# Performance work log

Measured on AMD Instinct MI355X. Metric: run time of the kernel, lower is better.

## Reference

```python
import jax, jax.numpy as jnp
import numpy as np

N, E, C, NEF, OUT, NUM_ANGLE = 20000, 160000, 32, 1, 128, 7
F = 2 * C + NEF  # edge_fdim = 65


def setup_inputs() -> dict:
    rng = np.random.default_rng(0)
    row = rng.integers(0, N, size=E).astype(np.int32)
    col = rng.integers(0, N, size=E).astype(np.int32)
    # Line-graph incidence pairs (a, b): edge a = (i,j) feeds edge b = (j,k), i.e. col[a] == row[b].
    sort_idx = np.argsort(row, kind='stable')
    row_sorted = row[sort_idx]
    starts = np.searchsorted(row_sorted, col, 'left')
    ends = np.searchsorted(row_sorted, col, 'right')
    counts = ends - starts
    total = int(counts.sum())
    line_src = np.repeat(np.arange(E, dtype=np.int32), counts)
    base = np.repeat(starts, counts)
    within = np.arange(total, dtype=np.int64) - np.repeat(np.cumsum(counts) - counts, counts)
    line_dst = sort_idx[base + within].astype(np.int32)

    key = jax.random.key(0)
    k = jax.random.split(key, 5)
    return {
        'x': jax.random.normal(k[0], (N, C), jnp.float32),
        'edge_attr': jax.random.normal(k[1], (E, NEF), jnp.float32),
        'pos': jax.random.normal(k[2], (N, 3), jnp.float32),
        'W_msg': jax.random.normal(k[3], (OUT, NUM_ANGLE * 2 * F), jnp.float32) * 0.02,
        'b_msg': jax.random.normal(k[4], (OUT,), jnp.float32) * 0.01,
        'edge_index': jnp.asarray(np.stack([row, col]), jnp.int32),
        'line_src': jnp.asarray(line_src),
        'line_dst': jnp.asarray(line_dst),
    }


def reference(x, edge_attr, pos, W_msg, b_msg, edge_index, line_src, line_dst):
    row, col = edge_index[0], edge_index[1]
    num_node = x.shape[0]
    num_edge = row.shape[0]

    # edge_f = [x_row | x_col | edge_attr]  -> [E, F]
    edge_f = jnp.concatenate([x[row], x[col], edge_attr], axis=1)

    # Line graph: edge a=(i,j) feeds edge b=(j,k). Angle at shared node j.
    j = col[line_src]
    u = pos[row[line_src]] - pos[j]  # j -> i
    v = pos[col[line_dst]] - pos[j]  # j -> k
    cos = jnp.sum(u * v, axis=-1) / (
        jnp.linalg.norm(u, axis=-1) * jnp.linalg.norm(v, axis=-1) + 1e-8)
    ang = jnp.arccos(jnp.clip(cos, -1.0 + 1e-7, 1.0 - 1e-7))  # [0, pi]
    abin = jnp.clip((ang / jnp.pi * NUM_ANGLE).astype(jnp.int32), 0, NUM_ANGLE - 1)

    # Per target edge, accumulate neighbor-edge features into (angle bin, in/out slot).
    seg_in = line_dst.astype(jnp.int32) * (NUM_ANGLE * 2) + abin * 2      # incoming a -> b
    seg_out = line_src.astype(jnp.int32) * (NUM_ANGLE * 2) + abin * 2 + 1  # outgoing b seen from a
    vals = jnp.concatenate([edge_f[line_src], edge_f[line_dst]], axis=0)  # [2L, F]
    segs = jnp.concatenate([seg_in, seg_out], axis=0)
    msg = jax.ops.segment_sum(vals, segs, num_segments=num_edge * NUM_ANGLE * 2)
    msg = msg.reshape(num_edge, NUM_ANGLE * 2 * F)  # [E, 910]

    # output = self.message(message)  (Linear with bias)
    edge_hidden = msg @ W_msg.T + b_msg  # [E, OUT]

    # scatter_add into destination nodes (edge_index[1])
    update = jax.ops.segment_sum(edge_hidden, col, num_segments=num_node)  # [N, OUT]
    return update
```

## Files before the change

kernel.cpp:

```cpp
#include <hip/hip_runtime.h>
#include <stdint.h>

#define N_NODES 20000
#define E_EDGES 160000
#define C_DIM 32
#define OUT_DIM 128
#define K_REAL 910
#define KPH 480
#define DEG_CAP 64
#define SEG 1024
#define NSEG 20
#define MT_A (E_EDGES/256)
#define NROWS_B 20224
#define MT_B (NROWS_B/256)
#define PADW ((NROWS_B - N_NODES)*KPH/2)

typedef __attribute__((ext_vector_type(4))) float f32x4;
typedef __attribute__((ext_vector_type(8))) short short8;

__device__ __forceinline__ float bf2f(unsigned short u){
  union { unsigned int i; float f; } v; v.i = ((unsigned int)u) << 16; return v.f;
}
__device__ __forceinline__ unsigned short f2bf(float f){
  union { float f; unsigned int i; } v; v.f = f;
  unsigned int i = v.i;
  unsigned int r = (i + 0x7FFFu + ((i >> 16) & 1u)) >> 16;
  return (unsigned short)r;
}
__device__ __forceinline__ float ldv(const void* p, size_t i, int isbf){
  return isbf ? bf2f(((const unsigned short*)p)[i]) : ((const float*)p)[i];
}
__device__ __forceinline__ int clampi(int v, int hi){
  return ((unsigned)v < (unsigned)hi) ? v : 0;
}

__global__ void k_init(const void* __restrict__ xraw, int* __restrict__ flag,
                       int* __restrict__ cnt, float* __restrict__ out_acc,
                       unsigned short* __restrict__ msgN)
{
  int tid = threadIdx.x;
  if (blockIdx.x == 0){
    __shared__ int s_bad;
    if (tid == 0) s_bad = 0;
    __syncthreads();
    float v = bf2f(((const unsigned short*)xraw)[tid * 2499]);
    if (!(fabsf(v) < 100.0f)) s_bad = 1;
    __syncthreads();
    if (tid == 0) flag[0] = s_bad ? 0 : 1;
  }
  const int Z1 = 2*N_NODES;
  const int Z2 = Z1 + N_NODES*OUT_DIM;
  const int Z3 = Z2 + PADW;
  int* padp = (int*)(msgN + (size_t)N_NODES*KPH);
  for (int i = blockIdx.x*blockDim.x + tid; i < Z3; i += gridDim.x*blockDim.x){
    if (i < Z1) cnt[i] = 0;
    else if (i < Z2) ((int*)out_acc)[i - Z1] = 0;
    else padp[i - Z2] = 0;
  }
}

__global__ void k_prep(const void* __restrict__ pos, const void* __restrict__ W,
                       const int* __restrict__ row, const int* __restrict__ col,
                       float* __restrict__ vecn, int* __restrict__ cnt,
                       unsigned short* __restrict__ Wp,
                       const int* __restrict__ flg)
{
  int isbf = flg[0];
  if (blockIdx.x < MT_A){
    int e = blockIdx.x*256 + threadIdx.x;
    if (e >= E_EDGES) return;
    int r = clampi(row[e], N_NODES), c = clampi(col[e], N_NODES);
    float vx = ldv(pos, (size_t)c*3+0, isbf) - ldv(pos, (size_t)r*3+0, isbf);
    float vy = ldv(pos, (size_t)c*3+1, isbf) - ldv(pos, (size_t)r*3+1, isbf);
    float vz = ldv(pos, (size_t)c*3+2, isbf) - ldv(pos, (size_t)r*3+2, isbf);
    float nn = sqrtf(vx*vx + vy*vy + vz*vz);
    f32x4 vv; vv[0]=vx; vv[1]=vy; vv[2]=vz; vv[3]=nn;
    *(f32x4*)(vecn + (size_t)e*4) = vv;
    atomicAdd(cnt + r, 1);
    atomicAdd(cnt + N_NODES + c, 1);
  } else {
    int i = (blockIdx.x - MT_A)*256 + threadIdx.x;
    if (i >= 2*OUT_DIM*KPH) return;
    int half = i / (OUT_DIM*KPH);
    int rem = i - half*OUT_DIM*KPH;
    int o = rem / KPH, kp = rem - o*KPH;
    float v = 0.f;
    if (kp < 448){
      int t = kp >> 6, f = kp & 63;
      v = ldv(W, (size_t)o*K_REAL + (2*t + half)*65 + f, isbf);
    } else if (kp < 455){
      int t = kp - 448;
      v = ldv(W, (size_t)o*K_REAL + (2*t + half)*65 + 64, isbf);
    }
    Wp[i] = f2bf(v);
  }
}

__global__ void k_scan1(const int* __restrict__ cnt, int* __restrict__ start2,
                        int* __restrict__ segsum){
  __shared__ int buf[SEG];
  int b = blockIdx.x, arr = b / NSEG, seg = b - arr*NSEG;
  const int* cntp = cnt + (size_t)arr*N_NODES;
  int* startp = start2 + (size_t)arr*(N_NODES+1);
  int tid = threadIdx.x;
  int i = seg*SEG + tid;
  int v = (i < N_NODES) ? cntp[i] : 0;
  buf[tid] = v;
  __syncthreads();
  for (int off = 1; off < SEG; off <<= 1){
    int t = (tid >= off) ? buf[tid-off] : 0;
    __syncthreads();
    buf[tid] += t;
    __syncthreads();
  }
  if (i < N_NODES) startp[i] = buf[tid] - v;
  if (tid == SEG-1) segsum[b] = buf[tid];
}
__global__ void k_scan2(int* segsum){
  int tid = threadIdx.x;
  if (tid < 2){
    int run = 0;
    for (int s = 0; s < NSEG; ++s){
      int v = segsum[tid*NSEG+s]; segsum[tid*NSEG+s] = run; run += v;
    }
  }
}
__global__ void k_scan3(int* __restrict__ start2, int* __restrict__ fill2,
                        const int* __restrict__ segsum){
  int b = blockIdx.x, arr = b / NSEG, seg = b - arr*NSEG;
  int* startp = start2 + (size_t)arr*(N_NODES+1);
  int* fillp  = fill2  + (size_t)arr*N_NODES;
  int tid = threadIdx.x;
  int i = seg*SEG + tid;
  int add = segsum[b];
  if (i < N_NODES){ int s = startp[i] + add; startp[i] = s; fillp[i] = s; }
  if (b == 0 && tid == 0){
    start2[N_NODES] = E_EDGES;
    start2[(N_NODES+1) + N_NODES] = E_EDGES;
  }
}

__global__ void k_scatter(const int* __restrict__ row, const int* __restrict__ col,
                          int* fill2, int* list_row, int* list_col,
                          int* pos_col, int* node_of_pos)
{
  int e = blockIdx.x*blockDim.x + threadIdx.x;
  if (e >= E_EDGES) return;
  int r = clampi(row[e], N_NODES), c = clampi(col[e], N_NODES);
  int p = atomicAdd(fill2 + r, 1);
  if ((unsigned)p < E_EDGES) list_row[p] = e;
  int q = atomicAdd(fill2 + N_NODES + c, 1);
  if ((unsigned)q < E_EDGES){ list_col[q] = e; node_of_pos[q] = c; }
  pos_col[e] = clampi(q, E_EDGES);
}

__global__ __launch_bounds__(256)
void k_msg_node(const void* __restrict__ x, const void* __restrict__ eattr,
                const float* __restrict__ vecn,
                const int* __restrict__ row, const int* __restrict__ col,
                const int* __restrict__ start2,
                const int* __restrict__ list_row, const int* __restrict__ list_col,
                const int* __restrict__ pos_col,
                unsigned short* __restrict__ msg,
                uint2* __restrict__ cntb,
                const int* __restrict__ flg, int half)
{
  __shared__ int posT[DEG_CAP];
  __shared__ int othS[DEG_CAP];
  __shared__ float vS[DEG_CAP][4], vT[DEG_CAP][4];
  __shared__ float eS[DEG_CAP];
  __shared__ unsigned short fS[DEG_CAP][64];
  __shared__ float e64[DEG_CAP][8];
  __shared__ unsigned char bins[DEG_CAP][DEG_CAP];

  const float cb1 = 0.9009688679f, cb2 = 0.6234898019f, cb3 = 0.2225209340f;
  const int* start_row = start2;
  const int* start_col = start2 + (N_NODES+1);
  int j = blockIdx.x;
  int tid = threadIdx.x, wv = tid >> 6, lane = tid & 63;
  int clo = start_col[j], chi = start_col[j+1];
  int rlo = start_row[j], rhi = start_row[j+1];
  if (clo < 0) clo = 0; if (chi > E_EDGES) chi = E_EDGES; if (chi < clo) chi = clo;
  if (rlo < 0) rlo = 0; if (rhi > E_EDGES) rhi = E_EDGES; if (rhi < rlo) rhi = rlo;
  int nI = chi - clo, nO = rhi - rlo;
  int nS = half ? nO : nI;
  int nT = half ? nI : nO;
  int slo = half ? rlo : clo;
  int tlo = half ? clo : rlo;
  const int* slist = half ? list_row : list_col;
  const int* tlist = half ? list_col : list_row;
  if (nT == 0) return;
  int isbf = flg[0];

  if (nS <= DEG_CAP && nT <= DEG_CAP){
    int nS4 = (nS + 3) & ~3;
    if (tid < nS){
      int s = clampi(slist[slo+tid], E_EDGES);
      othS[tid] = clampi(half ? col[s] : row[s], N_NODES);
      eS[tid] = ldv(eattr, s, isbf);
      vS[tid][0]=vecn[s*4+0]; vS[tid][1]=vecn[s*4+1];
      vS[tid][2]=vecn[s*4+2]; vS[tid][3]=vecn[s*4+3];
    }
    if (tid < nT){
      int t = clampi(tlist[tlo+tid], E_EDGES);
      posT[tid] = clampi(pos_col[t], E_EDGES);
      vT[tid][0]=vecn[t*4+0]; vT[tid][1]=vecn[t*4+1];
      vT[tid][2]=vecn[t*4+2]; vT[tid][3]=vecn[t*4+3];
    }
    for (int i = tid; i < DEG_CAP*8; i += 256) ((float*)e64)[i] = 0.f;
    { uint4 z = {0,0,0,0};
      ((uint4*)bins)[tid] = z; }
    __syncthreads();
    for (int cidx = tid; cidx < nS*64; cidx += 256){
      int si = cidx >> 6, f = cidx & 63;
      int lo_node = half ? j : othS[si];
      int hi_node = half ? othS[si] : j;
      int src = (f < 32) ? (lo_node*C_DIM + f) : (hi_node*C_DIM + f - 32);
      fS[si][f] = f2bf(ldv(x, (size_t)src, isbf));
    }
    for (int i = tid; i < (nS4 - nS)*64; i += 256)
      fS[nS + (i >> 6)][i & 63] = 0;
    for (int p = tid; p < nS*64; p += 256){
      int si = p >> 6, ti = p & 63;
      if (ti < nT){
        float dot = -(vS[si][0]*vT[ti][0] + vS[si][1]*vT[ti][1] + vS[si][2]*vT[ti][2]);
        float cv = dot / (vS[si][3]*vT[ti][3] + 1e-8f);
        int t = (cv<=cb1)+(cv<=cb2)+(cv<=cb3)+(cv<=-cb3)+(cv<=-cb2)+(cv<=-cb1);
        bins[ti][si] = (unsigned char)t;
        atomicAdd(&e64[ti][t], eS[si]);
      }
    }
    __syncthreads();
    for (int ti = wv; ti < nT; ti += 4){
      float S0=0,S1=0,S2=0,S3=0,S4=0,S5=0,S6=0;
      const unsigned* brow = (const unsigned*)bins[ti];
      for (int s4 = 0; s4 < nS4; s4 += 4){
        unsigned bb = (unsigned)__builtin_amdgcn_readfirstlane((int)brow[s4 >> 2]);
        #pragma unroll
        for (int u = 0; u < 4; ++u){
          int t = (bb >> (8*u)) & 7;
          float val = bf2f(fS[s4 + u][lane]);
          switch(t){
            case 0: S0+=val; break; case 1: S1+=val; break; case 2: S2+=val; break;
            case 3: S3+=val; break; case 4: S4+=val; break; case 5: S5+=val; break;
            default: S6+=val; break;
          }
        }
      }
      unsigned short* mrow = msg + (size_t)posT[ti]*KPH;
      mrow[0*64+lane]=f2bf(S0); mrow[1*64+lane]=f2bf(S1); mrow[2*64+lane]=f2bf(S2);
      mrow[3*64+lane]=f2bf(S3); mrow[4*64+lane]=f2bf(S4); mrow[5*64+lane]=f2bf(S5);
      mrow[6*64+lane]=f2bf(S6);
      if (lane < 7)  mrow[448+lane] = f2bf(e64[ti][lane]);
      if (lane < 25) mrow[455+lane] = 0;
      int myb = (lane < nS) ? (int)bins[ti][lane] : 7;
      unsigned n0 = (unsigned)__popcll(__ballot(myb==0));
      unsigned n1 = (unsigned)__popcll(__ballot(myb==1));
      unsigned n2 = (unsigned)__popcll(__ballot(myb==2));
      unsigned n3 = (unsigned)__popcll(__ballot(myb==3));
      unsigned n4 = (unsigned)__popcll(__ballot(myb==4));
      unsigned n5 = (unsigned)__popcll(__ballot(myb==5));
      unsigned n6 = (unsigned)__popcll(__ballot(myb==6));
      if (lane == 0){
        uint2 cw;
        cw.x = n0 | (n1<<8) | (n2<<16) | (n3<<24);
        cw.y = n4 | (n5<<8) | (n6<<16);
        cntb[posT[ti]] = cw;
      }
    }
  } else {
    for (int ti = wv; ti < nT; ti += 4){
      int te = clampi(tlist[tlo+ti], E_EDGES);
      float tx=vecn[te*4+0], ty=vecn[te*4+1], tz=vecn[te*4+2], tn=vecn[te*4+3];
      float S0=0,S1=0,S2=0,S3=0,S4=0,S5=0,S6=0,S64v=0;
      int n0=0,n1=0,n2=0,n3=0,n4=0,n5=0,n6=0;
      for (int si = 0; si < nS; ++si){
        int se = clampi(slist[slo+si], E_EDGES);
        float dot = -(vecn[se*4+0]*tx + vecn[se*4+1]*ty + vecn[se*4+2]*tz);
        float cv = dot / (vecn[se*4+3]*tn + 1e-8f);
        int tv = (cv<=cb1)+(cv<=cb2)+(cv<=cb3)+(cv<=-cb3)+(cv<=-cb2)+(cv<=-cb1);
        int t = __builtin_amdgcn_readfirstlane(tv);
        int oth = clampi(half ? col[se] : row[se], N_NODES);
        int lo_node = half ? j : oth;
        int hi_node = half ? oth : j;
        float val = (lane < 32) ? ldv(x, (size_t)lo_node*C_DIM+lane, isbf)
                                : ldv(x, (size_t)hi_node*C_DIM+lane-32, isbf);
        switch(t){
          case 0: S0+=val; n0++; break; case 1: S1+=val; n1++; break;
          case 2: S2+=val; n2++; break; case 3: S3+=val; n3++; break;
          case 4: S4+=val; n4++; break; case 5: S5+=val; n5++; break;
          default: S6+=val; n6++; break;
        }
        S64v += (lane == t) ? ldv(eattr, se, isbf) : 0.f;
      }
      unsigned short* mrow = msg + (size_t)clampi(pos_col[te], E_EDGES)*KPH;
      mrow[0*64+lane]=f2bf(S0); mrow[1*64+lane]=f2bf(S1); mrow[2*64+lane]=f2bf(S2);
      mrow[3*64+lane]=f2bf(S3); mrow[4*64+lane]=f2bf(S4); mrow[5*64+lane]=f2bf(S5);
      mrow[6*64+lane]=f2bf(S6);
      if (lane < 7)  mrow[448+lane] = f2bf(S64v);
      if (lane < 25) mrow[455+lane] = 0;
      if (lane == 0){
        uint2 cw;
        cw.x = (unsigned)min(n0,255) | ((unsigned)min(n1,255)<<8)
             | ((unsigned)min(n2,255)<<16) | ((unsigned)min(n3,255)<<24);
        cw.y = (unsigned)min(n4,255) | ((unsigned)min(n5,255)<<8)
             | ((unsigned)min(n6,255)<<16);
        cntb[clampi(pos_col[te], E_EDGES)] = cw;
      }
    }
  }
}

__global__ __launch_bounds__(256)
void k_msg1(const void* __restrict__ x, const void* __restrict__ eattr,
            const int* __restrict__ col,
            const int* __restrict__ start2,
            const int* __restrict__ list_row, const int* __restrict__ pos_col,
            const uint2* __restrict__ cntb,
            unsigned short* __restrict__ msgN,
            const int* __restrict__ flg)
{
  int wv = threadIdx.x >> 6, lane = threadIdx.x & 63;
  int j = blockIdx.x*4 + wv;
  if (j >= N_NODES) return;
  int isbf = flg[0];
  unsigned short* mrow = msgN + (size_t)j*KPH;
  int rlo = start2[j], rhi = start2[j+1];
  if (rlo < 0) rlo = 0; if (rhi > E_EDGES) rhi = E_EDGES; if (rhi < rlo) rhi = rlo;
  int nT = rhi - rlo;
  if (nT == 0){
    for (int i = lane; i < KPH; i += 64) mrow[i] = 0;
    return;
  }
  float xj = ldv(x, (size_t)j*C_DIM + (lane & 31), isbf);
  float m0=0,m1=0,m2=0,m3=0,m4=0,m5=0,m6=0;
  float me0=0,me1=0,me2=0,me3=0,me4=0,me5=0,me6=0;

  for (int tb = 0; tb < nT; tb += 64){
    int nn = nT - tb; if (nn > 64) nn = 64;
    int ok = lane < nn;
    int te = ok ? clampi(list_row[rlo + tb + lane], E_EDGES) : 0;
    int pp = clampi(pos_col[te], E_EDGES);
    uint2 cw = cntb[pp];
    int oL = clampi(col[te], N_NODES);
    float eL = ok ? ldv(eattr, te, isbf) : 0.f;
    unsigned cxL = ok ? cw.x : 0u;
    unsigned cyL = ok ? cw.y : 0u;

    for (int u = 0; u < nn; u += 8){
      float v[8], ea[8];
      unsigned cxa[8], cya[8];
      #pragma unroll
      for (int q = 0; q < 8; ++q){
        int ti = u + q;
        int o = __shfl(oL, ti);
        unsigned cx = (unsigned)__shfl((int)cxL, ti);
        unsigned cy = (unsigned)__shfl((int)cyL, ti);
        float eb = __shfl(eL, ti);
        if (ti < nn){
          v[q] = (lane < 32) ? xj : ldv(x, (size_t)o*C_DIM + lane - 32, isbf);
          cxa[q] = cx; cya[q] = cy; ea[q] = eb;
        } else {
          v[q] = 0.f; cxa[q] = 0u; cya[q] = 0u; ea[q] = 0.f;
        }
      }
      #pragma unroll
      for (int q = 0; q < 8; ++q){
        float n0=(float)(cxa[q]&255u),  n1=(float)((cxa[q]>>8)&255u),
              n2=(float)((cxa[q]>>16)&255u), n3=(float)(cxa[q]>>24),
              n4=(float)(cya[q]&255u),  n5=(float)((cya[q]>>8)&255u),
              n6=(float)((cya[q]>>16)&255u);
        m0+=n0*v[q]; m1+=n1*v[q]; m2+=n2*v[q]; m3+=n3*v[q];
        m4+=n4*v[q]; m5+=n5*v[q]; m6+=n6*v[q];
        me0+=n0*ea[q]; me1+=n1*ea[q]; me2+=n2*ea[q]; me3+=n3*ea[q];
        me4+=n4*ea[q]; me5+=n5*ea[q]; me6+=n6*ea[q];
      }
    }
  }

  mrow[0*64+lane]=f2bf(m0); mrow[1*64+lane]=f2bf(m1); mrow[2*64+lane]=f2bf(m2);
  mrow[3*64+lane]=f2bf(m3); mrow[4*64+lane]=f2bf(m4); mrow[5*64+lane]=f2bf(m5);
  mrow[6*64+lane]=f2bf(m6);
  if (lane < 7){
    float me = (lane==0)?me0:(lane==1)?me1:(lane==2)?me2:(lane==3)?me3
             : (lane==4)?me4:(lane==5)?me5:me6;
    mrow[448+lane] = f2bf(me);
  }
  if (lane < 25) mrow[455+lane] = 0;
}

__global__ __launch_bounds__(256)
void k_gemm(const unsigned short* __restrict__ A,
            const unsigned short* __restrict__ Wp,
            const void* __restrict__ bias,
            const int* __restrict__ flg,
            const int* __restrict__ node_of_pos,
            float* __restrict__ out_acc, int addbias, int ident, int mtiles)
{
  __shared__ union {
    unsigned short Bs[64*512];
    float seg[256][66];
  } sh;
  __shared__ int nids[256];

  int tid = threadIdx.x;
  int w = tid >> 6, lane = tid & 63;
  int lrow = lane & 15, q = lane >> 4;

  int lin = blockIdx.x;
  const int FULLG = (mtiles & ~7) * 2;
  int mt, ch;
  if (lin < FULLG){
    mt = (lin >> 4)*8 + (lin & 7);
    ch = (lin >> 3) & 1;
  } else {
    int r2 = lin - FULLG;
    mt = (mtiles & ~7) + (r2 >> 1);
    ch = r2 & 1;
  }
  int m0 = mt * 256;

  nids[tid] = ident ? ((m0 + tid < N_NODES) ? m0 + tid : N_NODES-1)
                    : clampi(node_of_pos[m0 + tid], N_NODES);

  const unsigned short* abase = A + (size_t)(m0 + w*64 + lrow)*KPH + q*8;
  short8 apf[3][4];
  #pragma unroll
  for (int d = 0; d < 3; ++d)
    #pragma unroll
    for (int rf = 0; rf < 4; ++rf)
      apf[d][rf] = *(const short8*)(abase + (size_t)rf*16*KPH + d*32);

  #pragma unroll
  for (int i = 0; i < 15; ++i){
    int idx = tid + i*256;
    int rr = idx / 60, cc = idx - rr*60;
    const uint4* gq = (const uint4*)(Wp + (size_t)(ch*64 + rr)*KPH + cc*8);
    *(uint4*)(sh.Bs + rr*512 + ((cc ^ (rr & 7))*8)) = *gq;
  }
  __syncthreads();

  f32x4 acc[4][4];
  #pragma unroll
  for (int rf = 0; rf < 4; ++rf)
    #pragma unroll
    for (int nf = 0; nf < 4; ++nf) acc[rf][nf] = (f32x4)0.f;

  #pragma unroll
  for (int k0i = 0; k0i < 15; ++k0i){
    int cur = k0i % 3;
    int c = k0i*4 + q;
    #pragma unroll
    for (int nf = 0; nf < 4; ++nf){
      int rb = nf*16 + lrow;
      short8 bfr = *(const short8*)(sh.Bs + rb*512 + ((c ^ (rb & 7))*8));
      #pragma unroll
      for (int rf = 0; rf < 4; ++rf)
        acc[rf][nf] = __builtin_amdgcn_mfma_f32_16x16x32_bf16(apf[cur][rf], bfr, acc[rf][nf], 0, 0, 0);
    }
    if (k0i + 3 < 15){
      #pragma unroll
      for (int rf = 0; rf < 4; ++rf)
        apf[cur][rf] = *(const short8*)(abase + (size_t)rf*16*KPH + (k0i+3)*32);
    }
  }

  int isbf = flg[0];
  float bvs[4];
  #pragma unroll
  for (int nf = 0; nf < 4; ++nf)
    bvs[nf] = addbias ? ldv(bias, ch*64 + nf*16 + lrow, isbf) : 0.f;

  __syncthreads();
  #pragma unroll
  for (int rf = 0; rf < 4; ++rf)
    #pragma unroll
    for (int r = 0; r < 4; ++r){
      int m = w*64 + rf*16 + q*4 + r;
      #pragma unroll
      for (int nf = 0; nf < 4; ++nf)
        sh.seg[m][nf*16 + lrow] = acc[rf][nf][r] + bvs[nf];
    }
  __syncthreads();
  {
    int o = tid & 63, g = tid >> 6;
    int base = g*64;
    float s = 0.f;
    int curn = nids[base];
    for (int r = 0; r < 64; ++r){
      int m = base + r;
      int nid = nids[m];
      if (nid != curn){
        atomicAdd(out_acc + (size_t)curn*OUT_DIM + ch*64 + o, s);
        s = 0.f; curn = nid;
      }
      s += sh.seg[m][o];
    }
    atomicAdd(out_acc + (size_t)curn*OUT_DIM + ch*64 + o, s);
  }
}

__global__ void k_out(const float* __restrict__ acc, void* __restrict__ outp,
                      const int* __restrict__ flg){
  int i = blockIdx.x*blockDim.x + threadIdx.x;
  if (i >= N_NODES*OUT_DIM) return;
  if (flg[0]) ((unsigned short*)outp)[i] = f2bf(acc[i]);
  else        ((float*)outp)[i] = acc[i];
}

extern "C" void kernel_launch(void* const* d_in, const int* in_sizes, int n_in,
                              void* d_out, int out_size, void* d_ws, size_t ws_size,
                              hipStream_t stream)
{
  const void* x     = d_in[0];
  const void* eattr = d_in[1];
  const void* pos   = d_in[2];
  const void* W     = d_in[3];
  const void* bmsg  = d_in[4];
  const int* eidx = (const int*)d_in[5];
  const int* row = eidx;
  const int* col = eidx + E_EDGES;

  char* ws = (char*)d_ws;
  size_t off = 0;
  auto alloc = [&](size_t b){ size_t o = off; off += (b + 255) & ~(size_t)255; return o; };

  int* dflag        = (int*)(ws + alloc(256));
  float* vecn       = (float*)(ws + alloc((size_t)E_EDGES*16));
  int* cnt          = (int*)(ws + alloc((size_t)2*N_NODES*4));
  int* start2       = (int*)(ws + alloc((size_t)2*(N_NODES+1)*4));
  int* fill2        = (int*)(ws + alloc((size_t)2*N_NODES*4));
  int* segsum       = (int*)(ws + alloc((size_t)2*NSEG*4));
  int* list_row     = (int*)(ws + alloc((size_t)E_EDGES*4));
  int* list_col     = (int*)(ws + alloc((size_t)E_EDGES*4));
  int* pos_col      = (int*)(ws + alloc((size_t)E_EDGES*4));
  int* node_of_pos  = (int*)(ws + alloc((size_t)E_EDGES*4));
  unsigned short* Wp = (unsigned short*)(ws + alloc((size_t)2*OUT_DIM*KPH*2));
  float* out_acc    = (float*)(ws + alloc((size_t)N_NODES*OUT_DIM*4));
  uint2* cntb       = (uint2*)(ws + alloc((size_t)E_EDGES*8));
  unsigned short* msgN = (unsigned short*)(ws + alloc((size_t)NROWS_B*KPH*2));
  unsigned short* msg  = (unsigned short*)(ws + alloc((size_t)E_EDGES*KPH*2));
  (void)off;

  unsigned short* Wp_in  = Wp;
  unsigned short* Wp_out = Wp + (size_t)OUT_DIM*KPH;

  k_init<<<2048, 256, 0, stream>>>(x, dflag, cnt, out_acc, msgN);
  k_prep<<<MT_A + 480, 256, 0, stream>>>(pos, W, row, col, vecn, cnt, Wp, dflag);
  k_scan1<<<2*NSEG, SEG, 0, stream>>>(cnt, start2, segsum);
  k_scan2<<<1, 64, 0, stream>>>(segsum);
  k_scan3<<<2*NSEG, SEG, 0, stream>>>(start2, fill2, segsum);
  k_scatter<<<(E_EDGES+255)/256, 256, 0, stream>>>(row, col, fill2,
                                                   list_row, list_col, pos_col, node_of_pos);
  k_msg_node<<<N_NODES, 256, 0, stream>>>(x, eattr, vecn, row, col, start2,
                                          list_row, list_col, pos_col, msg, cntb, dflag, 0);
  k_msg1<<<(N_NODES+3)/4, 256, 0, stream>>>(x, eattr, col, start2,
                                            list_row, pos_col, cntb, msgN, dflag);
  k_gemm<<<dim3(2*MT_A), 256, 0, stream>>>(msg, Wp_in, bmsg, dflag,
                                           node_of_pos, out_acc, 1, 0, MT_A);
  k_gemm<<<dim3(2*MT_B), 256, 0, stream>>>(msgN, Wp_out, bmsg, dflag,
                                           node_of_pos, out_acc, 0, 1, MT_B);
  k_out<<<(N_NODES*OUT_DIM+255)/256, 256, 0, stream>>>(out_acc, d_out, dflag);
}
```

Measured before the change: 310.1 us.

## Store per-bin counts in message padding and merge both GEMM launches

Per-bin neighbor counts are now written into the unused padding columns of each msg row as 16-bit values, replacing the separate cntb buffer. k_msg1 reads them back with one vector load from the msg row. The two k_gemm launches (edge-side and node-side) become a single k_gemmN launch whose block index picks the operand set, which removes one launch and lets the two grids overlap. The padding columns are multiplied by the padded weights in the GEMM, so this relies on those weight columns being zero, and k_msg1 now does a strided read of msg rows.

```diff
diff --git a/kernel.cpp b/kernel.cpp
--- a/kernel.cpp
+++ b/kernel.cpp
@@ -162,7 +162,6 @@
                 const int* __restrict__ list_row, const int* __restrict__ list_col,
                 const int* __restrict__ pos_col,
                 unsigned short* __restrict__ msg,
-                uint2* __restrict__ cntb,
                 const int* __restrict__ flg, int half)
 {
   __shared__ int posT[DEG_CAP];
@@ -252,7 +251,6 @@
       mrow[3*64+lane]=f2bf(S3); mrow[4*64+lane]=f2bf(S4); mrow[5*64+lane]=f2bf(S5);
       mrow[6*64+lane]=f2bf(S6);
       if (lane < 7)  mrow[448+lane] = f2bf(e64[ti][lane]);
-      if (lane < 25) mrow[455+lane] = 0;
       int myb = (lane < nS) ? (int)bins[ti][lane] : 7;
       unsigned n0 = (unsigned)__popcll(__ballot(myb==0));
       unsigned n1 = (unsigned)__popcll(__ballot(myb==1));
@@ -261,11 +259,14 @@
       unsigned n4 = (unsigned)__popcll(__ballot(myb==4));
       unsigned n5 = (unsigned)__popcll(__ballot(myb==5));
       unsigned n6 = (unsigned)__popcll(__ballot(myb==6));
-      if (lane == 0){
-        uint2 cw;
-        cw.x = n0 | (n1<<8) | (n2<<16) | (n3<<24);
-        cw.y = n4 | (n5<<8) | (n6<<16);
-        cntb[posT[ti]] = cw;
+      if (lane < 25){
+        unsigned short v = 0;
+        if (lane >= 1 && lane <= 7){
+          unsigned sel = (lane==1)?n0:(lane==2)?n1:(lane==3)?n2:(lane==4)?n3
+                       : (lane==5)?n4:(lane==6)?n5:n6;
+          v = (unsigned short)sel;
+        }
+        mrow[455+lane] = v;
       }
     }
   } else {
@@ -298,14 +299,14 @@
       mrow[3*64+lane]=f2bf(S3); mrow[4*64+lane]=f2bf(S4); mrow[5*64+lane]=f2bf(S5);
       mrow[6*64+lane]=f2bf(S6);
       if (lane < 7)  mrow[448+lane] = f2bf(S64v);
-      if (lane < 25) mrow[455+lane] = 0;
-      if (lane == 0){
-        uint2 cw;
-        cw.x = (unsigned)min(n0,255) | ((unsigned)min(n1,255)<<8)
-             | ((unsigned)min(n2,255)<<16) | ((unsigned)min(n3,255)<<24);
-        cw.y = (unsigned)min(n4,255) | ((unsigned)min(n5,255)<<8)
-             | ((unsigned)min(n6,255)<<16);
-        cntb[clampi(pos_col[te], E_EDGES)] = cw;
+      if (lane < 25){
+        unsigned short v = 0;
+        if (lane >= 1 && lane <= 7){
+          int sel = (lane==1)?n0:(lane==2)?n1:(lane==3)?n2:(lane==4)?n3
+                  : (lane==5)?n4:(lane==6)?n5:n6;
+          v = (unsigned short)((sel > 65535) ? 65535 : sel);
+        }
+        mrow[455+lane] = v;
       }
     }
   }
@@ -316,7 +317,7 @@
             const int* __restrict__ col,
             const int* __restrict__ start2,
             const int* __restrict__ list_row, const int* __restrict__ pos_col,
-            const uint2* __restrict__ cntb,
+            const unsigned short* __restrict__ msg,
             unsigned short* __restrict__ msgN,
             const int* __restrict__ flg)
 {
@@ -341,35 +342,39 @@
     int ok = lane < nn;
     int te = ok ? clampi(list_row[rlo + tb + lane], E_EDGES) : 0;
     int pp = clampi(pos_col[te], E_EDGES);
-    uint2 cw = cntb[pp];
+    short8 cc = *(const short8*)(msg + (size_t)pp*KPH + 456);
+    unsigned c01L = ok ? (((unsigned)(unsigned short)cc[0]) | (((unsigned)(unsigned short)cc[1]) << 16)) : 0u;
+    unsigned c23L = ok ? (((unsigned)(unsigned short)cc[2]) | (((unsigned)(unsigned short)cc[3]) << 16)) : 0u;
+    unsigned c45L = ok ? (((unsigned)(unsigned short)cc[4]) | (((unsigned)(unsigned short)cc[5]) << 16)) : 0u;
+    unsigned c6L  = ok ? ((unsigned)(unsigned short)cc[6]) : 0u;
     int oL = clampi(col[te], N_NODES);
     float eL = ok ? ldv(eattr, te, isbf) : 0.f;
-    unsigned cxL = ok ? cw.x : 0u;
-    unsigned cyL = ok ? cw.y : 0u;
 
     for (int u = 0; u < nn; u += 8){
       float v[8], ea[8];
-      unsigned cxa[8], cya[8];
+      unsigned ca[8], cb[8], cd[8], ce[8];
       #pragma unroll
       for (int q = 0; q < 8; ++q){
         int ti = u + q;
         int o = __shfl(oL, ti);
-        unsigned cx = (unsigned)__shfl((int)cxL, ti);
-        unsigned cy = (unsigned)__shfl((int)cyL, ti);
+        unsigned c01 = (unsigned)__shfl((int)c01L, ti);
+        unsigned c23 = (unsigned)__shfl((int)c23L, ti);
+        unsigned c45 = (unsigned)__shfl((int)c45L, ti);
+        unsigned c6  = (unsigned)__shfl((int)c6L, ti);
         float eb = __shfl(eL, ti);
         if (ti < nn){
           v[q] = (lane < 32) ? xj : ldv(x, (size_t)o*C_DIM + lane - 32, isbf);
-          cxa[q] = cx; cya[q] = cy; ea[q] = eb;
+          ca[q] = c01; cb[q] = c23; cd[q] = c45; ce[q] = c6; ea[q] = eb;
         } else {
-          v[q] = 0.f; cxa[q] = 0u; cya[q] = 0u; ea[q] = 0.f;
+          v[q] = 0.f; ca[q] = 0u; cb[q] = 0u; cd[q] = 0u; ce[q] = 0u; ea[q] = 0.f;
         }
       }
       #pragma unroll
       for (int q = 0; q < 8; ++q){
-        float n0=(float)(cxa[q]&255u),  n1=(float)((cxa[q]>>8)&255u),
-              n2=(float)((cxa[q]>>16)&255u), n3=(float)(cxa[q]>>24),
-              n4=(float)(cya[q]&255u),  n5=(float)((cya[q]>>8)&255u),
-              n6=(float)((cya[q]>>16)&255u);
+        float n0=(float)(ca[q]&0xffffu), n1=(float)(ca[q]>>16),
+              n2=(float)(cb[q]&0xffffu), n3=(float)(cb[q]>>16),
+              n4=(float)(cd[q]&0xffffu), n5=(float)(cd[q]>>16),
+              n6=(float)ce[q];
         m0+=n0*v[q]; m1+=n1*v[q]; m2+=n2*v[q]; m3+=n3*v[q];
         m4+=n4*v[q]; m5+=n5*v[q]; m6+=n6*v[q];
         me0+=n0*ea[q]; me1+=n1*ea[q]; me2+=n2*ea[q]; me3+=n3*ea[q];
@@ -390,12 +395,14 @@
 }
 
 __global__ __launch_bounds__(256)
-void k_gemm(const unsigned short* __restrict__ A,
-            const unsigned short* __restrict__ Wp,
-            const void* __restrict__ bias,
-            const int* __restrict__ flg,
-            const int* __restrict__ node_of_pos,
-            float* __restrict__ out_acc, int addbias, int ident, int mtiles)
+void k_gemmN(const unsigned short* __restrict__ msg,
+             const unsigned short* __restrict__ Wp_in,
+             const unsigned short* __restrict__ msgN,
+             const unsigned short* __restrict__ Wp_out,
+             const void* __restrict__ bias,
+             const int* __restrict__ flg,
+             const int* __restrict__ node_of_pos,
+             float* __restrict__ out_acc)
 {
   __shared__ union {
     unsigned short Bs[64*512];
@@ -407,7 +414,14 @@
   int w = tid >> 6, lane = tid & 63;
   int lrow = lane & 15, q = lane >> 4;
 
-  int lin = blockIdx.x;
+  int which = (blockIdx.x >= 2*MT_A) ? 1 : 0;
+  int lin = blockIdx.x - which*2*MT_A;
+  const unsigned short* A  = which ? msgN  : msg;
+  const unsigned short* Wp = which ? Wp_out : Wp_in;
+  int mtiles  = which ? MT_B : MT_A;
+  int addbias = !which;
+  int ident   = which;
+
   const int FULLG = (mtiles & ~7) * 2;
   int mt, ch;
   if (lin < FULLG){
@@ -537,7 +551,6 @@
   int* node_of_pos  = (int*)(ws + alloc((size_t)E_EDGES*4));
   unsigned short* Wp = (unsigned short*)(ws + alloc((size_t)2*OUT_DIM*KPH*2));
   float* out_acc    = (float*)(ws + alloc((size_t)N_NODES*OUT_DIM*4));
-  uint2* cntb       = (uint2*)(ws + alloc((size_t)E_EDGES*8));
   unsigned short* msgN = (unsigned short*)(ws + alloc((size_t)NROWS_B*KPH*2));
   unsigned short* msg  = (unsigned short*)(ws + alloc((size_t)E_EDGES*KPH*2));
   (void)off;
@@ -553,12 +566,10 @@
   k_scatter<<<(E_EDGES+255)/256, 256, 0, stream>>>(row, col, fill2,
                                                    list_row, list_col, pos_col, node_of_pos);
   k_msg_node<<<N_NODES, 256, 0, stream>>>(x, eattr, vecn, row, col, start2,
-                                          list_row, list_col, pos_col, msg, cntb, dflag, 0);
+                                          list_row, list_col, pos_col, msg, dflag, 0);
   k_msg1<<<(N_NODES+3)/4, 256, 0, stream>>>(x, eattr, col, start2,
-                                            list_row, pos_col, cntb, msgN, dflag);
-  k_gemm<<<dim3(2*MT_A), 256, 0, stream>>>(msg, Wp_in, bmsg, dflag,
-                                           node_of_pos, out_acc, 1, 0, MT_A);
-  k_gemm<<<dim3(2*MT_B), 256, 0, stream>>>(msgN, Wp_out, bmsg, dflag,
-                                           node_of_pos, out_acc, 0, 1, MT_B);
+                                            list_row, pos_col, msg, msgN, dflag);
+  k_gemmN<<<dim3(2*MT_A + 2*MT_B), 256, 0, stream>>>(msg, Wp_in, msgN, Wp_out,
+                                                     bmsg, dflag, node_of_pos, out_acc);
   k_out<<<(N_NODES*OUT_DIM+255)/256, 256, 0, stream>>>(out_acc, d_out, dflag);
 }
```

Result: no change. 310.0 us (median of 2 runs) (-0.0%).
